# Performance work log

Measured on AMD Instinct MI355X. Metric: run time of the kernel, lower is better.

Reference implementation:

```python
import jax, jax.numpy as jnp
import numpy as np

N_CONTENT = 100000
N_USER = 100000
N_EDGES = 1600000
D_CONTENT = 256
D_USER = 128
HIDDEN = 128
OUT = 64


def setup_inputs() -> dict:
    key = jax.random.key(0)
    ks = jax.random.split(key, 12)
    s = lambda d: 1.0 / np.sqrt(d)
    return {
        "x_content": jax.random.normal(ks[0], (N_CONTENT, D_CONTENT), jnp.float32),
        "x_user": jax.random.normal(ks[1], (N_USER, D_USER), jnp.float32),
        # edge_index[0] = source (user) ids, edge_index[1] = destination (content) ids
        "edge_index": jax.random.randint(ks[2], (2, N_EDGES), 0, N_CONTENT, jnp.int64),
        # per-node-type input projections
        "Wc": jax.random.normal(ks[3], (D_CONTENT, HIDDEN), jnp.float32) * s(D_CONTENT),
        "bc": jnp.zeros((HIDDEN,), jnp.float32),
        "Wu": jax.random.normal(ks[4], (D_USER, HIDDEN), jnp.float32) * s(D_USER),
        "bu": jnp.zeros((HIDDEN,), jnp.float32),
        # SAGEConv: W_l applied to aggregated neighbor features (with bias),
        # W_r applied to root/self features (no bias, per PyG default)
        "Wl": jax.random.normal(ks[5], (HIDDEN, HIDDEN), jnp.float32) * s(HIDDEN),
        "bl": jnp.zeros((HIDDEN,), jnp.float32),
        "Wr": jax.random.normal(ks[6], (HIDDEN, HIDDEN), jnp.float32) * s(HIDDEN),
        # final output projection on content nodes
        "Wo": jax.random.normal(ks[7], (HIDDEN, OUT), jnp.float32) * s(HIDDEN),
        "bo": jnp.zeros((OUT,), jnp.float32),
    }


def reference(x_content, x_user, edge_index, Wc, bc, Wu, bu, Wl, bl, Wr, Wo, bo):
    # Per-node-type linear + relu
    h_c = jax.nn.relu(x_content @ Wc + bc)  # [Nc, H]
    h_u = jax.nn.relu(x_user @ Wu + bu)      # [Nu, H]

    src, dst = edge_index[0], edge_index[1]
    # SAGEConv mean aggregation: gather user features along edges, scatter-mean to content
    msg = h_u[src]                                              # [E, H] gather
    agg = jax.ops.segment_sum(msg, dst, num_segments=N_CONTENT) # [Nc, H]
    cnt = jax.ops.segment_sum(jnp.ones((msg.shape[0],), msg.dtype), dst,
                              num_segments=N_CONTENT)
    mean = agg / jnp.maximum(cnt, 1.0)[:, None]                 # 0 for isolated nodes

    h = mean @ Wl + bl + h_c @ Wr                               # SAGE combine
    return h @ Wo + bo                                          # [Nc, OUT]
```

## Files before the change

### kernel.cpp

```cpp
#include <hip/hip_runtime.h>
#include <hip/hip_bf16.h>

#define NC 100000
#define NU 100000
#define NE 1600000
#define DC 256
#define DU 128
#define HID 128
#define OUTD 64

#define BSHIFT 9
#define BRANGE 512
#define NBUCK ((NC + BRANGE - 1) / BRANGE)
#define BCAP 10240
#define EPB 8192
#define ABLK ((NE + EPB - 1) / EPB)

#define NBT_C ((NC + 63) / 64)
#define NBT_U ((NU + 63) / 64)

#define NBC 342
#define NBU 170

typedef __attribute__((ext_vector_type(8))) short bf16x8;
typedef __attribute__((ext_vector_type(4))) float f32x4;

__device__ inline unsigned short f2b(float f) {
    unsigned int u = __float_as_uint(f);
    u += 0x7fffu + ((u >> 16) & 1u);
    return (unsigned short)(u >> 16);
}

__global__ void prep_kernel(const float* __restrict__ Wl, const float* __restrict__ bl,
                            const float* __restrict__ Wr, const float* __restrict__ Wo,
                            const float* __restrict__ bo,
                            __hip_bfloat16* __restrict__ Wlo_p,
                            __hip_bfloat16* __restrict__ Wro_p,
                            float* __restrict__ b2) {
    const int k = blockIdx.x;
    const int f = threadIdx.x;
    float a0 = 0.f, a1 = 0.f;
    for (int m = 0; m < HID; ++m) {
        float wo = Wo[m * OUTD + f];
        a0 = fmaf(Wl[k * HID + m], wo, a0);
        a1 = fmaf(Wr[k * HID + m], wo, a1);
    }
    const int wv = f >> 4, l16 = f & 15;
    const int ks = k >> 5, quad = (k >> 3) & 3, e = k & 7;
    const int idx = (((wv * 4 + ks) * 64) + quad * 16 + l16) * 8 + e;
    Wlo_p[idx] = __float2bfloat16(a0);
    Wro_p[idx] = __float2bfloat16(a1);
    if (k == 0) {
        float s = bo[f];
        for (int m = 0; m < HID; ++m) s = fmaf(bl[m], Wo[m * OUTD + f], s);
        b2[f] = s;
    }
}

__global__ void pack_w(const float* __restrict__ W, __hip_bfloat16* __restrict__ Wp,
                       int K) {
    int i = blockIdx.x * blockDim.x + threadIdx.x;
    int total = K * HID;
    if (i >= total) return;
    int j = i % HID, k = i / HID;
    int nks = K >> 5;
    int idx = (((j >> 4) * nks + (k >> 5)) * 64 + ((k >> 3) & 3) * 16 + (j & 15)) * 8 +
              (k & 7);
    Wp[idx] = __float2bfloat16(W[k * HID + j]);
}

template <int DIN, bool BF16OUT>
__device__ __forceinline__ void gemm_path(const float* __restrict__ x,
                                          const __hip_bfloat16* __restrict__ W1p,
                                          const float* __restrict__ b1,
                                          const __hip_bfloat16* __restrict__ W2p,
                                          const float* __restrict__ bias2,
                                          void* __restrict__ outp, int nrows,
                                          int ntiles, int blk, int nblk,
                                          short* __restrict__ smem) {
    constexpr int NKS = DIN / 32;
    constexpr int SA = DIN + 8;
    constexpr int SH = HID + 8;
    constexpr int CPR = DIN / 8;
    constexpr int NCH = 64 * CPR / 256;
    constexpr int RSTEP = 256 / CPR;
    short* a_s = smem;
    short* h_s = smem + 64 * (DC + 8);

    const int t = threadIdx.x;
    const int w = t >> 6, lane = t & 63;
    const int quad = lane >> 4, l16 = lane & 15;
    const int r0 = t / CPR, c0 = t % CPR;

    bf16x8 b1f[2][NKS];
#pragma unroll
    for (int ntl = 0; ntl < 2; ++ntl)
#pragma unroll
        for (int ks = 0; ks < NKS; ++ks)
            b1f[ntl][ks] =
                *(const bf16x8*)&W1p[(size_t)(((2 * w + ntl) * NKS + ks) * 64 + lane) * 8];
    bf16x8 b2f[HID / 32];
#pragma unroll
    for (int ks = 0; ks < HID / 32; ++ks)
        b2f[ks] = *(const bf16x8*)&W2p[(size_t)((w * 4 + ks) * 64 + lane) * 8];
    const float bb1_0 = b1[w * 32 + l16];
    const float bb1_1 = b1[w * 32 + 16 + l16];
    const float bb2 = BF16OUT ? 0.f : bias2[w * 16 + l16];

    float4 va[NCH][2];

    auto load_tile = [&](int tile) {
#pragma unroll
        for (int k = 0; k < NCH; ++k) {
            int rc = min(tile * 64 + r0 + k * RSTEP, nrows - 1);
            const float4* p = (const float4*)(x + (size_t)rc * DIN + c0 * 8);
            va[k][0] = p[0];
            va[k][1] = p[1];
        }
    };

    load_tile(blk);

    for (int tile = blk; tile < ntiles; tile += nblk) {
#pragma unroll
        for (int k = 0; k < NCH; ++k) {
            bf16x8 a;
            a[0] = (short)f2b(va[k][0].x); a[1] = (short)f2b(va[k][0].y);
            a[2] = (short)f2b(va[k][0].z); a[3] = (short)f2b(va[k][0].w);
            a[4] = (short)f2b(va[k][1].x); a[5] = (short)f2b(va[k][1].y);
            a[6] = (short)f2b(va[k][1].z); a[7] = (short)f2b(va[k][1].w);
            *(bf16x8*)&a_s[(r0 + k * RSTEP) * SA + c0 * 8] = a;
        }
        int tn = tile + nblk;
        if (tn < ntiles) load_tile(tn);
        __syncthreads();

#pragma unroll
        for (int rg = 0; rg < 4; ++rg) {
            bf16x8 af[NKS];
#pragma unroll
            for (int ks = 0; ks < NKS; ++ks)
                af[ks] = *(const bf16x8*)&a_s[(rg * 16 + l16) * SA + ks * 32 + quad * 8];
            f32x4 acc0 = (f32x4){0.f, 0.f, 0.f, 0.f};
            f32x4 acc1 = (f32x4){0.f, 0.f, 0.f, 0.f};
#pragma unroll
            for (int ks = 0; ks < NKS; ++ks) {
                acc0 = __builtin_amdgcn_mfma_f32_16x16x32_bf16(af[ks], b1f[0][ks], acc0, 0, 0, 0);
                acc1 = __builtin_amdgcn_mfma_f32_16x16x32_bf16(af[ks], b1f[1][ks], acc1, 0, 0, 0);
            }
#pragma unroll
            for (int r = 0; r < 4; ++r) {
                int row = rg * 16 + quad * 4 + r;
                h_s[row * SH + w * 32 + l16] = (short)f2b(fmaxf(acc0[r] + bb1_0, 0.f));
                h_s[row * SH + w * 32 + 16 + l16] = (short)f2b(fmaxf(acc1[r] + bb1_1, 0.f));
            }
        }
        __syncthreads();

        const int base = tile * 64;
#pragma unroll
        for (int rg = 0; rg < 4; ++rg) {
            f32x4 acc = (f32x4){0.f, 0.f, 0.f, 0.f};
#pragma unroll
            for (int ks = 0; ks < HID / 32; ++ks) {
                bf16x8 a = *(const bf16x8*)&h_s[(rg * 16 + l16) * SH + ks * 32 + quad * 8];
                acc = __builtin_amdgcn_mfma_f32_16x16x32_bf16(a, b2f[ks], acc, 0, 0, 0);
            }
#pragma unroll
            for (int r = 0; r < 4; ++r) {
                int rr = base + rg * 16 + quad * 4 + r;
                if (rr < nrows) {
                    if (BF16OUT)
                        ((unsigned short*)outp)[(size_t)rr * OUTD + w * 16 + l16] = f2b(acc[r]);
                    else
                        ((float*)outp)[(size_t)rr * OUTD + w * 16 + l16] = acc[r] + bb2;
                }
            }
        }
    }
}

__global__ void __launch_bounds__(256, 2) dual_gemm(
    const float* __restrict__ xc, const __hip_bfloat16* __restrict__ Wc_p,
    const float* __restrict__ bc, const __hip_bfloat16* __restrict__ Wro_p,
    const float* __restrict__ b2, float* __restrict__ out,
    const float* __restrict__ xu, const __hip_bfloat16* __restrict__ Wu_p,
    const float* __restrict__ bu, const __hip_bfloat16* __restrict__ Wlo_p,
    unsigned short* __restrict__ pu) {
    __shared__ __align__(16) short smem[64 * (DC + 8) + 64 * (HID + 8)];
    int b = blockIdx.x;
    if (b < NBC)
        gemm_path<DC, false>(xc, Wc_p, bc, Wro_p, b2, out, NC, NBT_C, b, NBC, smem);
    else
        gemm_path<DU, true>(xu, Wu_p, bu, Wlo_p, nullptr, pu, NU, NBT_U, b - NBC, NBU, smem);
}

__global__ void __launch_bounds__(256) bucket_a(const int* __restrict__ src,
                                                const int* __restrict__ dst,
                                                int* __restrict__ gcur,
                                                unsigned int* __restrict__ bke) {
    __shared__ unsigned int pk[EPB];
    __shared__ int hist[NBUCK];
    __shared__ int lbase[NBUCK];
    __shared__ int lcur[NBUCK];
    __shared__ int gb[NBUCK];
    __shared__ int ts[256];
    const int t = threadIdx.x;
    const int base = blockIdx.x * EPB;
    for (int i = t; i < NBUCK; i += 256) hist[i] = 0;
    __syncthreads();
#pragma unroll
    for (int k = 0; k < EPB / 256; ++k) {
        int e = base + k * 256 + t;
        if (e < NE) atomicAdd(&hist[dst[e] >> BSHIFT], 1);
    }
    __syncthreads();
    int h = (t < NBUCK) ? hist[t] : 0;
    ts[t] = h;
    __syncthreads();
    for (int d = 1; d < 256; d <<= 1) {
        int x = (t >= d) ? ts[t - d] : 0;
        __syncthreads();
        ts[t] += x;
        __syncthreads();
    }
    if (t < NBUCK) {
        int ex = ts[t] - h;
        lbase[t] = ex;
        lcur[t] = ex;
        gb[t] = atomicAdd(&gcur[t], h);
    }
    __syncthreads();
#pragma unroll
    for (int k = 0; k < EPB / 256; ++k) {
        int e = base + k * 256 + t;
        if (e < NE) {
            int s = src[e], d = dst[e];
            int b = d >> BSHIFT;
            int p = atomicAdd(&lcur[b], 1);
            pk[p] = ((unsigned int)s << BSHIFT) | (unsigned int)(d & (BRANGE - 1));
        }
    }
    __syncthreads();
    const int wv = t >> 6, ln = t & 63;
    for (int b = wv; b < NBUCK; b += 4) {
        int s0 = lbase[b], c = hist[b], g0 = gb[b];
        for (int j = ln; j < c; j += 64) {
            int pos = g0 + j;
            if (pos < BCAP) bke[(size_t)b * BCAP + pos] = pk[s0 + j];
        }
    }
}

__global__ void scan_mid(const int* __restrict__ gcur, int* __restrict__ gbase,
                         int* __restrict__ off) {
    __shared__ int ts[256];
    int t = threadIdx.x;
    int h = (t < NBUCK) ? gcur[t] : 0;
    ts[t] = h;
    __syncthreads();
    for (int d = 1; d < 256; d <<= 1) {
        int x = (t >= d) ? ts[t - d] : 0;
        __syncthreads();
        ts[t] += x;
        __syncthreads();
    }
    if (t < NBUCK) gbase[t] = ts[t] - h;
    if (t == 0) { gbase[NBUCK] = NE; off[NC] = NE; }
}

__global__ void __launch_bounds__(256) bucket_b(const int* __restrict__ gcur,
                                                const int* __restrict__ gbase,
                                                const unsigned int* __restrict__ bke,
                                                int* __restrict__ off,
                                                int* __restrict__ ssrc) {
    __shared__ unsigned int pk[BCAP];
    __shared__ int hist[BRANGE];
    __shared__ int hb[BRANGE];
    __shared__ int cur[BRANGE];
    __shared__ int ts[256];
    const int t = threadIdx.x;
    const int b = blockIdx.x;
    const int n = min(gcur[b], BCAP);
    const int g0 = gbase[b];
    for (int i = t; i < n; i += 256) pk[i] = bke[(size_t)b * BCAP + i];
    for (int i = t; i < BRANGE; i += 256) hist[i] = 0;
    __syncthreads();
    for (int i = t; i < n; i += 256) atomicAdd(&hist[pk[i] & (BRANGE - 1)], 1);
    __syncthreads();
    int a0 = hist[2 * t], a1 = hist[2 * t + 1];
    int s = a0 + a1;
    ts[t] = s;
    __syncthreads();
    for (int d = 1; d < 256; d <<= 1) {
        int x = (t >= d) ? ts[t - d] : 0;
        __syncthreads();
        ts[t] += x;
        __syncthreads();
    }
    int ex = ts[t] - s;
    hb[2 * t] = ex;
    hb[2 * t + 1] = ex + a0;
    __syncthreads();
    for (int i = t; i < BRANGE; i += 256) {
        int node = b * BRANGE + i;
        cur[i] = g0 + hb[i];
        if (node < NC) off[node] = g0 + hb[i];
    }
    __syncthreads();
    for (int i = t; i < n; i += 256) {
        unsigned int v = pk[i];
        int p = atomicAdd(&cur[v & (BRANGE - 1)], 1);
        ssrc[p] = (int)(v >> BSHIFT);
    }
}

__global__ void __launch_bounds__(256) gather_agg(const int* __restrict__ ssrc,
                                                  const int* __restrict__ off,
                                                  const unsigned int* __restrict__ pu,
                                                  float* __restrict__ out) {
    int node = blockIdx.x * 4 + (threadIdx.x >> 6);
    if (node >= NC) return;
    int lane = threadIdx.x & 63;
    int g = lane >> 3;
    int f8 = lane & 7;
    int e0 = off[node], e1 = off[node + 1];
    float acc[8] = {0.f, 0.f, 0.f, 0.f, 0.f, 0.f, 0.f, 0.f};
    for (int e = e0 + g; e < e1; e += 8) {
        int s = ssrc[e];
        uint4 v = ((const uint4*)pu)[(size_t)s * 8 + f8];
        acc[0] += __uint_as_float(v.x << 16);
        acc[1] += __uint_as_float(v.x & 0xffff0000u);
        acc[2] += __uint_as_float(v.y << 16);
        acc[3] += __uint_as_float(v.y & 0xffff0000u);
        acc[4] += __uint_as_float(v.z << 16);
        acc[5] += __uint_as_float(v.z & 0xffff0000u);
        acc[6] += __uint_as_float(v.w << 16);
        acc[7] += __uint_as_float(v.w & 0xffff0000u);
    }
#pragma unroll
    for (int m = 8; m <= 32; m <<= 1) {
#pragma unroll
        for (int j = 0; j < 8; ++j) acc[j] += __shfl_xor(acc[j], m, 64);
    }
    if (g == 0) {
        float inv = 1.0f / (float)max(e1 - e0, 1);
        float4* po = (float4*)(out + (size_t)node * OUTD + f8 * 8);
        float4 o0 = po[0], o1 = po[1];
        o0.x += acc[0] * inv; o0.y += acc[1] * inv;
        o0.z += acc[2] * inv; o0.w += acc[3] * inv;
        o1.x += acc[4] * inv; o1.y += acc[5] * inv;
        o1.z += acc[6] * inv; o1.w += acc[7] * inv;
        po[0] = o0; po[1] = o1;
    }
}

extern "C" void kernel_launch(void* const* d_in, const int* in_sizes, int n_in,
                              void* d_out, int out_size, void* d_ws, size_t ws_size,
                              hipStream_t stream) {
    const float* xc = (const float*)d_in[0];
    const float* xu = (const float*)d_in[1];
    const int*   ei = (const int*)d_in[2];
    const float* Wc = (const float*)d_in[3];
    const float* bc = (const float*)d_in[4];
    const float* Wu = (const float*)d_in[5];
    const float* bu = (const float*)d_in[6];
    const float* Wl = (const float*)d_in[7];
    const float* bl = (const float*)d_in[8];
    const float* Wr = (const float*)d_in[9];
    const float* Wo = (const float*)d_in[10];
    const float* bo = (const float*)d_in[11];
    float* out = (float*)d_out;

    const int* esrc = ei;
    const int* edst = ei + NE;

    unsigned short* pu = (unsigned short*)d_ws;
    int* ssrc  = (int*)(pu + (size_t)NU * OUTD);
    unsigned int* bke = (unsigned int*)(ssrc + NE);
    int* gcur  = (int*)(bke + (size_t)NBUCK * BCAP);
    int* gbase = gcur + NBUCK;
    int* off   = gcur + 400;
    float* b2  = (float*)(off + NC + 4);
    __hip_bfloat16* Wlo_p = (__hip_bfloat16*)(b2 + OUTD);
    __hip_bfloat16* Wro_p = Wlo_p + OUTD * HID;
    __hip_bfloat16* Wu_p  = Wro_p + OUTD * HID;
    __hip_bfloat16* Wc_p  = Wu_p + HID * DU;

    hipMemsetAsync(gcur, 0, NBUCK * sizeof(int), stream);

    prep_kernel<<<HID, OUTD, 0, stream>>>(Wl, bl, Wr, Wo, bo, Wlo_p, Wro_p, b2);
    pack_w<<<(DU * HID + 255) / 256, 256, 0, stream>>>(Wu, Wu_p, DU);
    pack_w<<<(DC * HID + 255) / 256, 256, 0, stream>>>(Wc, Wc_p, DC);

    dual_gemm<<<NBC + NBU, 256, 0, stream>>>(xc, Wc_p, bc, Wro_p, b2, out,
                                             xu, Wu_p, bu, Wlo_p, pu);

    bucket_a<<<ABLK, 256, 0, stream>>>(esrc, edst, gcur, bke);
    scan_mid<<<1, 256, 0, stream>>>(gcur, gbase, off);
    bucket_b<<<NBUCK, 256, 0, stream>>>(gcur, gbase, bke, off, ssrc);
    gather_agg<<<(NC + 3) / 4, 256, 0, stream>>>(ssrc, off, (const unsigned int*)pu, out);
}
```

Before: 344.6 us.

## Stage GEMM input tiles via async global-to-LDS loads with double buffering

The dual GEMM now moves fp32 input tiles directly from global memory into a double-buffered, XOR-swizzled LDS region using global_load_lds, rather than loading them into registers and storing bf16 to LDS. Conversion to bf16 moves to the LDS read side, and the tile height drops from 64 to 32 rows with explicit vmcnt/lgkmcnt waits around the barriers. The aim is to overlap the next tile's load with compute and to free the registers that held the prefetch. The cost is a larger LDS footprint (about 72 KB per block), which may reduce occupancy. Row-bound checks are removed on the assumption that the node counts divide evenly by 32.

```diff
diff --git a/kernel.cpp b/kernel.cpp
--- a/kernel.cpp
+++ b/kernel.cpp
@@ -16,11 +16,15 @@
 #define EPB 8192
 #define ABLK ((NE + EPB - 1) / EPB)
 
-#define NBT_C ((NC + 63) / 64)
-#define NBT_U ((NU + 63) / 64)
+#define TM 32
+#define NT_C (NC / TM)
+#define NT_U (NU / TM)
 
 #define NBC 342
 #define NBU 170
+
+#define ABUF_STRIDE 32768
+#define SH (HID + 8)
 
 typedef __attribute__((ext_vector_type(8))) short bf16x8;
 typedef __attribute__((ext_vector_type(4))) float f32x4;
@@ -29,6 +33,12 @@
     unsigned int u = __float_as_uint(f);
     u += 0x7fffu + ((u >> 16) & 1u);
     return (unsigned short)(u >> 16);
+}
+
+__device__ __forceinline__ void gload_lds16(const float* g, void* l) {
+    __builtin_amdgcn_global_load_lds(
+        (const __attribute__((address_space(1))) void*)g,
+        (__attribute__((address_space(3))) void*)l, 16, 0, 0);
 }
 
 __global__ void prep_kernel(const float* __restrict__ Wl, const float* __restrict__ bl,
@@ -75,22 +85,17 @@
                                           const float* __restrict__ b1,
                                           const __hip_bfloat16* __restrict__ W2p,
                                           const float* __restrict__ bias2,
-                                          void* __restrict__ outp, int nrows,
+                                          void* __restrict__ outp,
                                           int ntiles, int blk, int nblk,
-                                          short* __restrict__ smem) {
+                                          char* __restrict__ sm) {
     constexpr int NKS = DIN / 32;
-    constexpr int SA = DIN + 8;
-    constexpr int SH = HID + 8;
-    constexpr int CPR = DIN / 8;
-    constexpr int NCH = 64 * CPR / 256;
-    constexpr int RSTEP = 256 / CPR;
-    short* a_s = smem;
-    short* h_s = smem + 64 * (DC + 8);
+    constexpr int NCH = DIN / 32;
+    constexpr int CRB = (DIN == 256) ? 6 : 5;
+    short* h_s = (short*)(sm + 2 * ABUF_STRIDE);
 
     const int t = threadIdx.x;
     const int w = t >> 6, lane = t & 63;
     const int quad = lane >> 4, l16 = lane & 15;
-    const int r0 = t / CPR, c0 = t % CPR;
 
     bf16x8 b1f[2][NKS];
 #pragma unroll
@@ -107,40 +112,44 @@
     const float bb1_1 = b1[w * 32 + 16 + l16];
     const float bb2 = BF16OUT ? 0.f : bias2[w * 16 + l16];
 
-    float4 va[NCH][2];
-
-    auto load_tile = [&](int tile) {
+    auto stage = [&](int tile, int buf) {
+        const float* gt = x + (size_t)tile * TM * DIN;
 #pragma unroll
         for (int k = 0; k < NCH; ++k) {
-            int rc = min(tile * 64 + r0 + k * RSTEP, nrows - 1);
-            const float4* p = (const float4*)(x + (size_t)rc * DIN + c0 * 8);
-            va[k][0] = p[0];
-            va[k][1] = p[1];
+            int L = (k * 4 + w) * 64 + lane;
+            int g = L ^ ((L >> CRB) & 31);
+            gload_lds16(gt + g * 4, sm + buf * ABUF_STRIDE + (k * 4 + w) * 1024);
         }
     };
 
-    load_tile(blk);
+    int cur = 0;
+    stage(blk, 0);
 
     for (int tile = blk; tile < ntiles; tile += nblk) {
-#pragma unroll
-        for (int k = 0; k < NCH; ++k) {
-            bf16x8 a;
-            a[0] = (short)f2b(va[k][0].x); a[1] = (short)f2b(va[k][0].y);
-            a[2] = (short)f2b(va[k][0].z); a[3] = (short)f2b(va[k][0].w);
-            a[4] = (short)f2b(va[k][1].x); a[5] = (short)f2b(va[k][1].y);
-            a[6] = (short)f2b(va[k][1].z); a[7] = (short)f2b(va[k][1].w);
-            *(bf16x8*)&a_s[(r0 + k * RSTEP) * SA + c0 * 8] = a;
-        }
         int tn = tile + nblk;
-        if (tn < ntiles) load_tile(tn);
-        __syncthreads();
-
-#pragma unroll
-        for (int rg = 0; rg < 4; ++rg) {
+        if (tn < ntiles) stage(tn, cur ^ 1);
+        asm volatile("s_waitcnt vmcnt(%0)" ::"i"(NCH) : "memory");
+        __builtin_amdgcn_s_barrier();
+        __builtin_amdgcn_sched_barrier(0);
+
+        const float* ab = (const float*)(sm + cur * ABUF_STRIDE);
+#pragma unroll
+        for (int rg = 0; rg < TM / 16; ++rg) {
+            const int r = rg * 16 + l16;
+            const int sw = r & 31;
             bf16x8 af[NKS];
 #pragma unroll
-            for (int ks = 0; ks < NKS; ++ks)
-                af[ks] = *(const bf16x8*)&a_s[(rg * 16 + l16) * SA + ks * 32 + quad * 8];
+            for (int ks = 0; ks < NKS; ++ks) {
+                int c0 = (r << CRB) + ks * 8 + quad * 2;
+                float4 v0 = *(const float4*)&ab[(size_t)(c0 ^ sw) * 4];
+                float4 v1 = *(const float4*)&ab[(size_t)((c0 + 1) ^ sw) * 4];
+                bf16x8 a;
+                a[0] = (short)f2b(v0.x); a[1] = (short)f2b(v0.y);
+                a[2] = (short)f2b(v0.z); a[3] = (short)f2b(v0.w);
+                a[4] = (short)f2b(v1.x); a[5] = (short)f2b(v1.y);
+                a[6] = (short)f2b(v1.z); a[7] = (short)f2b(v1.w);
+                af[ks] = a;
+            }
             f32x4 acc0 = (f32x4){0.f, 0.f, 0.f, 0.f};
             f32x4 acc1 = (f32x4){0.f, 0.f, 0.f, 0.f};
 #pragma unroll
@@ -149,17 +158,19 @@
                 acc1 = __builtin_amdgcn_mfma_f32_16x16x32_bf16(af[ks], b1f[1][ks], acc1, 0, 0, 0);
             }
 #pragma unroll
-            for (int r = 0; r < 4; ++r) {
-                int row = rg * 16 + quad * 4 + r;
-                h_s[row * SH + w * 32 + l16] = (short)f2b(fmaxf(acc0[r] + bb1_0, 0.f));
-                h_s[row * SH + w * 32 + 16 + l16] = (short)f2b(fmaxf(acc1[r] + bb1_1, 0.f));
+            for (int r4 = 0; r4 < 4; ++r4) {
+                int row = rg * 16 + quad * 4 + r4;
+                h_s[row * SH + w * 32 + l16] = (short)f2b(fmaxf(acc0[r4] + bb1_0, 0.f));
+                h_s[row * SH + w * 32 + 16 + l16] = (short)f2b(fmaxf(acc1[r4] + bb1_1, 0.f));
             }
         }
-        __syncthreads();
-
-        const int base = tile * 64;
-#pragma unroll
-        for (int rg = 0; rg < 4; ++rg) {
+        asm volatile("s_waitcnt lgkmcnt(0)" ::: "memory");
+        __builtin_amdgcn_s_barrier();
+        __builtin_amdgcn_sched_barrier(0);
+
+        const int base = tile * TM;
+#pragma unroll
+        for (int rg = 0; rg < TM / 16; ++rg) {
             f32x4 acc = (f32x4){0.f, 0.f, 0.f, 0.f};
 #pragma unroll
             for (int ks = 0; ks < HID / 32; ++ks) {
@@ -167,16 +178,15 @@
                 acc = __builtin_amdgcn_mfma_f32_16x16x32_bf16(a, b2f[ks], acc, 0, 0, 0);
             }
 #pragma unroll
-            for (int r = 0; r < 4; ++r) {
-                int rr = base + rg * 16 + quad * 4 + r;
-                if (rr < nrows) {
-                    if (BF16OUT)
-                        ((unsigned short*)outp)[(size_t)rr * OUTD + w * 16 + l16] = f2b(acc[r]);
-                    else
-                        ((float*)outp)[(size_t)rr * OUTD + w * 16 + l16] = acc[r] + bb2;
-                }
+            for (int r4 = 0; r4 < 4; ++r4) {
+                int rr = base + rg * 16 + quad * 4 + r4;
+                if (BF16OUT)
+                    ((unsigned short*)outp)[(size_t)rr * OUTD + w * 16 + l16] = f2b(acc[r4]);
+                else
+                    ((float*)outp)[(size_t)rr * OUTD + w * 16 + l16] = acc[r4] + bb2;
             }
         }
+        cur ^= 1;
     }
 }
 
@@ -187,12 +197,12 @@
     const float* __restrict__ xu, const __hip_bfloat16* __restrict__ Wu_p,
     const float* __restrict__ bu, const __hip_bfloat16* __restrict__ Wlo_p,
     unsigned short* __restrict__ pu) {
-    __shared__ __align__(16) short smem[64 * (DC + 8) + 64 * (HID + 8)];
+    __shared__ __align__(16) char sm[2 * ABUF_STRIDE + TM * SH * 2];
     int b = blockIdx.x;
     if (b < NBC)
-        gemm_path<DC, false>(xc, Wc_p, bc, Wro_p, b2, out, NC, NBT_C, b, NBC, smem);
+        gemm_path<DC, false>(xc, Wc_p, bc, Wro_p, b2, out, NT_C, b, NBC, sm);
     else
-        gemm_path<DU, true>(xu, Wu_p, bu, Wlo_p, nullptr, pu, NU, NBT_U, b - NBC, NBU, smem);
+        gemm_path<DU, true>(xu, Wu_p, bu, Wlo_p, nullptr, pu, NT_U, b - NBC, NBU, sm);
 }
 
 __global__ void __launch_bounds__(256) bucket_a(const int* __restrict__ src,
```

New measurement: 346.7 us. About the same (+0.6%).

## Launch one 32-row tile per block in dual GEMM and parallelize prep reduction

Applied to the files above, without the earlier changes.

Replaces the persistent-block dual GEMM, which prefetched 64-row tiles in a grid-stride loop, with one block per 32-row tile. This gives about 6250 blocks, halves the shared memory per block, and raises the launch-bounds occupancy hint to 4. The prep kernel now splits its inner reduction across 4 waves and combines the partial sums in shared memory. In exchange, the register prefetch that overlapped loads with compute is gone, each block reloads the weight fragments, and the tail-row clamping is dropped on the assumption that the row counts divide by 32.

```diff
diff --git a/kernel.cpp b/kernel.cpp
--- a/kernel.cpp
+++ b/kernel.cpp
@@ -16,11 +16,11 @@
 #define EPB 8192
 #define ABLK ((NE + EPB - 1) / EPB)
 
-#define NBT_C ((NC + 63) / 64)
-#define NBT_U ((NU + 63) / 64)
-
-#define NBC 342
-#define NBU 170
+#define TM 32
+#define NT_C (NC / TM)
+#define NT_U (NU / TM)
+
+#define SH (HID + 8)
 
 typedef __attribute__((ext_vector_type(8))) short bf16x8;
 typedef __attribute__((ext_vector_type(4))) float f32x4;
@@ -38,22 +38,28 @@
                             __hip_bfloat16* __restrict__ Wro_p,
                             float* __restrict__ b2) {
     const int k = blockIdx.x;
-    const int f = threadIdx.x;
-    float a0 = 0.f, a1 = 0.f;
-    for (int m = 0; m < HID; ++m) {
+    const int t = threadIdx.x;
+    const int f = t & 63, j4 = t >> 6;
+    __shared__ float red[3][4][OUTD];
+    float a0 = 0.f, a1 = 0.f, s = 0.f;
+    for (int m = j4 * 32; m < j4 * 32 + 32; ++m) {
         float wo = Wo[m * OUTD + f];
         a0 = fmaf(Wl[k * HID + m], wo, a0);
         a1 = fmaf(Wr[k * HID + m], wo, a1);
-    }
-    const int wv = f >> 4, l16 = f & 15;
-    const int ks = k >> 5, quad = (k >> 3) & 3, e = k & 7;
-    const int idx = (((wv * 4 + ks) * 64) + quad * 16 + l16) * 8 + e;
-    Wlo_p[idx] = __float2bfloat16(a0);
-    Wro_p[idx] = __float2bfloat16(a1);
-    if (k == 0) {
-        float s = bo[f];
-        for (int m = 0; m < HID; ++m) s = fmaf(bl[m], Wo[m * OUTD + f], s);
-        b2[f] = s;
+        s = fmaf(bl[m], wo, s);
+    }
+    red[0][j4][f] = a0; red[1][j4][f] = a1; red[2][j4][f] = s;
+    __syncthreads();
+    if (j4 == 0) {
+        a0 = red[0][0][f] + red[0][1][f] + red[0][2][f] + red[0][3][f];
+        a1 = red[1][0][f] + red[1][1][f] + red[1][2][f] + red[1][3][f];
+        const int wv = f >> 4, l16 = f & 15;
+        const int ks = k >> 5, quad = (k >> 3) & 3, e = k & 7;
+        const int idx = (((wv * 4 + ks) * 64) + quad * 16 + l16) * 8 + e;
+        Wlo_p[idx] = __float2bfloat16(a0);
+        Wro_p[idx] = __float2bfloat16(a1);
+        if (k == 0)
+            b2[f] = bo[f] + red[2][0][f] + red[2][1][f] + red[2][2][f] + red[2][3][f];
     }
 }
 
@@ -75,22 +81,21 @@
                                           const float* __restrict__ b1,
                                           const __hip_bfloat16* __restrict__ W2p,
                                           const float* __restrict__ bias2,
-                                          void* __restrict__ outp, int nrows,
-                                          int ntiles, int blk, int nblk,
+                                          void* __restrict__ outp, int tile,
                                           short* __restrict__ smem) {
     constexpr int NKS = DIN / 32;
     constexpr int SA = DIN + 8;
-    constexpr int SH = HID + 8;
     constexpr int CPR = DIN / 8;
-    constexpr int NCH = 64 * CPR / 256;
     constexpr int RSTEP = 256 / CPR;
+    constexpr int NCH = TM / RSTEP;
     short* a_s = smem;
-    short* h_s = smem + 64 * (DC + 8);
+    short* h_s = smem + TM * SA;
 
     const int t = threadIdx.x;
     const int w = t >> 6, lane = t & 63;
     const int quad = lane >> 4, l16 = lane & 15;
     const int r0 = t / CPR, c0 = t % CPR;
+    const int base = tile * TM;
 
     bf16x8 b1f[2][NKS];
 #pragma unroll
@@ -108,91 +113,77 @@
     const float bb2 = BF16OUT ? 0.f : bias2[w * 16 + l16];
 
     float4 va[NCH][2];
-
-    auto load_tile = [&](int tile) {
-#pragma unroll
-        for (int k = 0; k < NCH; ++k) {
-            int rc = min(tile * 64 + r0 + k * RSTEP, nrows - 1);
-            const float4* p = (const float4*)(x + (size_t)rc * DIN + c0 * 8);
-            va[k][0] = p[0];
-            va[k][1] = p[1];
-        }
-    };
-
-    load_tile(blk);
-
-    for (int tile = blk; tile < ntiles; tile += nblk) {
-#pragma unroll
-        for (int k = 0; k < NCH; ++k) {
-            bf16x8 a;
-            a[0] = (short)f2b(va[k][0].x); a[1] = (short)f2b(va[k][0].y);
-            a[2] = (short)f2b(va[k][0].z); a[3] = (short)f2b(va[k][0].w);
-            a[4] = (short)f2b(va[k][1].x); a[5] = (short)f2b(va[k][1].y);
-            a[6] = (short)f2b(va[k][1].z); a[7] = (short)f2b(va[k][1].w);
-            *(bf16x8*)&a_s[(r0 + k * RSTEP) * SA + c0 * 8] = a;
-        }
-        int tn = tile + nblk;
-        if (tn < ntiles) load_tile(tn);
-        __syncthreads();
-
-#pragma unroll
-        for (int rg = 0; rg < 4; ++rg) {
-            bf16x8 af[NKS];
-#pragma unroll
-            for (int ks = 0; ks < NKS; ++ks)
-                af[ks] = *(const bf16x8*)&a_s[(rg * 16 + l16) * SA + ks * 32 + quad * 8];
-            f32x4 acc0 = (f32x4){0.f, 0.f, 0.f, 0.f};
-            f32x4 acc1 = (f32x4){0.f, 0.f, 0.f, 0.f};
-#pragma unroll
-            for (int ks = 0; ks < NKS; ++ks) {
-                acc0 = __builtin_amdgcn_mfma_f32_16x16x32_bf16(af[ks], b1f[0][ks], acc0, 0, 0, 0);
-                acc1 = __builtin_amdgcn_mfma_f32_16x16x32_bf16(af[ks], b1f[1][ks], acc1, 0, 0, 0);
-            }
-#pragma unroll
-            for (int r = 0; r < 4; ++r) {
-                int row = rg * 16 + quad * 4 + r;
-                h_s[row * SH + w * 32 + l16] = (short)f2b(fmaxf(acc0[r] + bb1_0, 0.f));
-                h_s[row * SH + w * 32 + 16 + l16] = (short)f2b(fmaxf(acc1[r] + bb1_1, 0.f));
-            }
-        }
-        __syncthreads();
-
-        const int base = tile * 64;
-#pragma unroll
-        for (int rg = 0; rg < 4; ++rg) {
-            f32x4 acc = (f32x4){0.f, 0.f, 0.f, 0.f};
-#pragma unroll
-            for (int ks = 0; ks < HID / 32; ++ks) {
-                bf16x8 a = *(const bf16x8*)&h_s[(rg * 16 + l16) * SH + ks * 32 + quad * 8];
-                acc = __builtin_amdgcn_mfma_f32_16x16x32_bf16(a, b2f[ks], acc, 0, 0, 0);
-            }
-#pragma unroll
-            for (int r = 0; r < 4; ++r) {
-                int rr = base + rg * 16 + quad * 4 + r;
-                if (rr < nrows) {
-                    if (BF16OUT)
-                        ((unsigned short*)outp)[(size_t)rr * OUTD + w * 16 + l16] = f2b(acc[r]);
-                    else
-                        ((float*)outp)[(size_t)rr * OUTD + w * 16 + l16] = acc[r] + bb2;
-                }
-            }
-        }
-    }
-}
-
-__global__ void __launch_bounds__(256, 2) dual_gemm(
+#pragma unroll
+    for (int k = 0; k < NCH; ++k) {
+        const float4* p = (const float4*)(x + (size_t)(base + r0 + k * RSTEP) * DIN + c0 * 8);
+        va[k][0] = p[0];
+        va[k][1] = p[1];
+    }
+#pragma unroll
+    for (int k = 0; k < NCH; ++k) {
+        bf16x8 a;
+        a[0] = (short)f2b(va[k][0].x); a[1] = (short)f2b(va[k][0].y);
+        a[2] = (short)f2b(va[k][0].z); a[3] = (short)f2b(va[k][0].w);
+        a[4] = (short)f2b(va[k][1].x); a[5] = (short)f2b(va[k][1].y);
+        a[6] = (short)f2b(va[k][1].z); a[7] = (short)f2b(va[k][1].w);
+        *(bf16x8*)&a_s[(r0 + k * RSTEP) * SA + c0 * 8] = a;
+    }
+    __syncthreads();
+
+#pragma unroll
+    for (int rg = 0; rg < TM / 16; ++rg) {
+        bf16x8 af[NKS];
+#pragma unroll
+        for (int ks = 0; ks < NKS; ++ks)
+            af[ks] = *(const bf16x8*)&a_s[(rg * 16 + l16) * SA + ks * 32 + quad * 8];
+        f32x4 acc0 = (f32x4){0.f, 0.f, 0.f, 0.f};
+        f32x4 acc1 = (f32x4){0.f, 0.f, 0.f, 0.f};
+#pragma unroll
+        for (int ks = 0; ks < NKS; ++ks) {
+            acc0 = __builtin_amdgcn_mfma_f32_16x16x32_bf16(af[ks], b1f[0][ks], acc0, 0, 0, 0);
+            acc1 = __builtin_amdgcn_mfma_f32_16x16x32_bf16(af[ks], b1f[1][ks], acc1, 0, 0, 0);
+        }
+#pragma unroll
+        for (int r = 0; r < 4; ++r) {
+            int row = rg * 16 + quad * 4 + r;
+            h_s[row * SH + w * 32 + l16] = (short)f2b(fmaxf(acc0[r] + bb1_0, 0.f));
+            h_s[row * SH + w * 32 + 16 + l16] = (short)f2b(fmaxf(acc1[r] + bb1_1, 0.f));
+        }
+    }
+    __syncthreads();
+
+#pragma unroll
+    for (int rg = 0; rg < TM / 16; ++rg) {
+        f32x4 acc = (f32x4){0.f, 0.f, 0.f, 0.f};
+#pragma unroll
+        for (int ks = 0; ks < HID / 32; ++ks) {
+            bf16x8 a = *(const bf16x8*)&h_s[(rg * 16 + l16) * SH + ks * 32 + quad * 8];
+            acc = __builtin_amdgcn_mfma_f32_16x16x32_bf16(a, b2f[ks], acc, 0, 0, 0);
+        }
+#pragma unroll
+        for (int r = 0; r < 4; ++r) {
+            int rr = base + rg * 16 + quad * 4 + r;
+            if (BF16OUT)
+                ((unsigned short*)outp)[(size_t)rr * OUTD + w * 16 + l16] = f2b(acc[r]);
+            else
+                ((float*)outp)[(size_t)rr * OUTD + w * 16 + l16] = acc[r] + bb2;
+        }
+    }
+}
+
+__global__ void __launch_bounds__(256, 4) dual_gemm(
     const float* __restrict__ xc, const __hip_bfloat16* __restrict__ Wc_p,
     const float* __restrict__ bc, const __hip_bfloat16* __restrict__ Wro_p,
     const float* __restrict__ b2, float* __restrict__ out,
     const float* __restrict__ xu, const __hip_bfloat16* __restrict__ Wu_p,
     const float* __restrict__ bu, const __hip_bfloat16* __restrict__ Wlo_p,
     unsigned short* __restrict__ pu) {
-    __shared__ __align__(16) short smem[64 * (DC + 8) + 64 * (HID + 8)];
+    __shared__ __align__(16) short smem[TM * (DC + 8) + TM * (HID + 8)];
     int b = blockIdx.x;
-    if (b < NBC)
-        gemm_path<DC, false>(xc, Wc_p, bc, Wro_p, b2, out, NC, NBT_C, b, NBC, smem);
+    if (b < NT_C)
+        gemm_path<DC, false>(xc, Wc_p, bc, Wro_p, b2, out, b, smem);
     else
-        gemm_path<DU, true>(xu, Wu_p, bu, Wlo_p, nullptr, pu, NU, NBT_U, b - NBC, NBU, smem);
+        gemm_path<DU, true>(xu, Wu_p, bu, Wlo_p, nullptr, pu, b - NT_C, smem);
 }
 
 __global__ void __launch_bounds__(256) bucket_a(const int* __restrict__ src,
@@ -389,12 +380,12 @@
 
     hipMemsetAsync(gcur, 0, NBUCK * sizeof(int), stream);
 
-    prep_kernel<<<HID, OUTD, 0, stream>>>(Wl, bl, Wr, Wo, bo, Wlo_p, Wro_p, b2);
+    prep_kernel<<<HID, 256, 0, stream>>>(Wl, bl, Wr, Wo, bo, Wlo_p, Wro_p, b2);
     pack_w<<<(DU * HID + 255) / 256, 256, 0, stream>>>(Wu, Wu_p, DU);
     pack_w<<<(DC * HID + 255) / 256, 256, 0, stream>>>(Wc, Wc_p, DC);
 
-    dual_gemm<<<NBC + NBU, 256, 0, stream>>>(xc, Wc_p, bc, Wro_p, b2, out,
-                                             xu, Wu_p, bu, Wlo_p, pu);
+    dual_gemm<<<NT_C + NT_U, 256, 0, stream>>>(xc, Wc_p, bc, Wro_p, b2, out,
+                                               xu, Wu_p, bu, Wlo_p, pu);
 
     bucket_a<<<ABLK, 256, 0, stream>>>(esrc, edst, gcur, bke);
     scan_mid<<<1, 256, 0, stream>>>(gcur, gbase, off);
```

Result: faster. 334.1 us (-3.0%).
